# Kernel optimization log

Hardware: AMD Instinct MI355X
Metric: run time of the kernel (lower is better)

Reference implementation:

```python
import jax, jax.numpy as jnp
import numpy as np

B, N, M, K = 4, 2048, 8192, 3          # batches, coarse pts/batch, fine pts/batch, knn k
C_IN, C_SKIP, H, C_OUT = 256, 128, 256, 128


def setup_inputs() -> dict:
    key = jax.random.key(0)
    ks = jax.random.split(key, 8)
    x = jax.random.normal(ks[0], (B * N, C_IN), jnp.float32)
    pos = jax.random.normal(ks[1], (B * N, 3), jnp.float32)
    batch = jnp.repeat(jnp.arange(B, dtype=jnp.int64), N)        # sorted, equal-sized batches
    x_skip = jax.random.normal(ks[2], (B * M, C_SKIP), jnp.float32)
    pos_skip = jax.random.normal(ks[3], (B * M, 3), jnp.float32)
    batch_skip = jnp.repeat(jnp.arange(B, dtype=jnp.int64), M)
    # MLP params: Linear(384->256) + ReLU + Linear(256->128)
    W1 = jax.random.normal(ks[4], (C_IN + C_SKIP, H), jnp.float32) / np.sqrt(C_IN + C_SKIP)
    b1 = jnp.zeros((H,), jnp.float32)
    W2 = jax.random.normal(ks[5], (H, C_OUT), jnp.float32) / np.sqrt(H)
    b2 = jnp.zeros((C_OUT,), jnp.float32)
    return {"x": x, "pos": pos, "x_skip": x_skip, "pos_skip": pos_skip,
            "W1": W1, "b1": b1, "W2": W2, "b2": b2,
            "batch": batch, "batch_skip": batch_skip}


def _knn_interpolate(x, pos, pos_skip):
    # x: [B*N, C], pos: [B*N, 3], pos_skip: [B*M, 3]; batches are equal-sized & sorted,
    # so per-batch kNN == reshape to [B, n, ...] (matches batch/batch_skip vectors).
    xb = x.reshape(B, N, C_IN)
    pb = pos.reshape(B, N, 3)
    qb = pos_skip.reshape(B, M, 3)
    # squared pairwise distances via GEMM expansion: [B, M, N]
    d2 = (jnp.sum(qb * qb, -1)[:, :, None]
          + jnp.sum(pb * pb, -1)[:, None, :]
          - 2.0 * jnp.einsum('bmd,bnd->bmn', qb, pb))
    neg_d2, idx = jax.lax.top_k(-d2, K)           # k smallest distances
    d2k = jnp.maximum(-neg_d2, 0.0)               # [B, M, K]
    w = 1.0 / (d2k + 1e-16)                       # inverse-squared-distance weights
    feats = xb[jnp.arange(B)[:, None, None], idx] # gather: [B, M, K, C]
    interp = jnp.sum(w[..., None] * feats, axis=2) / jnp.sum(w, axis=2)[..., None]
    return interp.reshape(B * M, C_IN)


def reference(x, pos, x_skip, pos_skip, W1, b1, W2, b2, batch, batch_skip):
    xi = _knn_interpolate(x, pos, pos_skip)              # [B*M, C_IN]
    h = jnp.concatenate([xi, x_skip], axis=1)            # [B*M, C_IN+C_SKIP]
    h = jax.nn.relu(h @ W1 + b1)
    out = h @ W2 + b2                                    # [B*M, C_OUT]
    return (out, pos_skip, batch_skip)
```

## Files before the change

kernel.cpp:

```cpp
#include <hip/hip_runtime.h>
#include <math.h>
#include <stdint.h>

#define Bn    4
#define Nn    2048
#define Mn    8192
#define CIN   256
#define CSKIP 128
#define HID   256
#define COUT  128
#define KTOT  384

typedef short bf16x8 __attribute__((ext_vector_type(8)));
typedef float f32x16 __attribute__((ext_vector_type(16)));

__device__ __forceinline__ ushort f2bf(float f) {
    union { float f; unsigned u; } v; v.f = f;
    return (ushort)((v.u + 0x7fffu + ((v.u >> 16) & 1u)) >> 16);
}
__device__ __forceinline__ float bf2f(ushort u) {
    union { unsigned u; float f; } v; v.u = ((unsigned)u) << 16;
    return v.f;
}

#define INSERT3(kA, kB, kC, k)            \
    do {                                  \
        const double _t = fmax(kA, k);    \
        kA = fmin(kA, k);                 \
        const double _u = fmax(kB, _t);   \
        kB = fmin(kB, _t);                \
        kC = fmin(kC, _u);                \
    } while (0)

__global__ __launch_bounds__(256) void prep_kernel(
    const float* __restrict__ x, const float* __restrict__ xs,
    const float* __restrict__ pos, const float* __restrict__ pos_skip,
    const float* __restrict__ W1, const float* __restrict__ W2,
    ushort* __restrict__ xb, ushort* __restrict__ xsb,
    ushort* __restrict__ W1T, ushort* __restrict__ W2T,
    float4* __restrict__ pos4, float* __restrict__ tail_dst)
{
    const int bid = blockIdx.x, tid = threadIdx.x;
    if (bid < 2048) {
        const int q   = bid * 256 + tid;
        const int row = q >> 6;
        const int cq  = (q & 63) * 4;
        const float4 v = *(const float4*)(x + (size_t)row * CIN + cq);
        ushort4 o; o.x = f2bf(v.x); o.y = f2bf(v.y); o.z = f2bf(v.z); o.w = f2bf(v.w);
        *(ushort4*)(xb + (size_t)row * CIN + cq) = o;
    } else if (bid < 6144) {
        const int q   = (bid - 2048) * 256 + tid;
        const int row = q >> 5;
        const int cq  = (q & 31) * 4;
        const float4 v = *(const float4*)(xs + (size_t)row * CSKIP + cq);
        ushort4 o; o.x = f2bf(v.x); o.y = f2bf(v.y); o.z = f2bf(v.z); o.w = f2bf(v.w);
        *(ushort4*)(xsb + (size_t)row * CSKIP + cq) = o;
    } else if (bid < 6240) {
        const int q  = (bid - 6144) * 256 + tid;
        const int n  = q / 96;
        const int kq = (q % 96) * 4;
        ushort4 o;
        o.x = f2bf(W1[(size_t)(kq + 0) * HID + n]);
        o.y = f2bf(W1[(size_t)(kq + 1) * HID + n]);
        o.z = f2bf(W1[(size_t)(kq + 2) * HID + n]);
        o.w = f2bf(W1[(size_t)(kq + 3) * HID + n]);
        *(ushort4*)(W1T + (size_t)n * KTOT + kq) = o;
    } else if (bid < 6272) {
        const int q  = (bid - 6240) * 256 + tid;
        const int n  = q >> 6;
        const int kq = (q & 63) * 4;
        ushort4 o;
        o.x = f2bf(W2[(size_t)(kq + 0) * COUT + n]);
        o.y = f2bf(W2[(size_t)(kq + 1) * COUT + n]);
        o.z = f2bf(W2[(size_t)(kq + 2) * COUT + n]);
        o.w = f2bf(W2[(size_t)(kq + 3) * COUT + n]);
        *(ushort4*)(W2T + (size_t)n * HID + kq) = o;
    } else if (bid < 6304) {
        const int i = (bid - 6272) * 256 + tid;
        const float* p = pos + (size_t)i * 3;
        const float p0 = p[0], p1 = p[1], p2 = p[2];
        const float pp = __fadd_rn(__fadd_rn(__fmul_rn(p0, p0), __fmul_rn(p1, p1)),
                                   __fmul_rn(p2, p2));
        pos4[i] = make_float4(2.0f * p0, 2.0f * p1, 2.0f * p2, pp);
    } else {
        const int i = (bid - 6304) * 256 + tid;
        const int nPos = Bn * Mn * 3;
        if (i < nPos) tail_dst[i] = pos_skip[i];
        else          tail_dst[i] = (float)((i - nPos) >> 13);
    }
}

__device__ __forceinline__ void gemm_acc128(
    const ushort* __restrict__ A, int lda,
    const ushort* __restrict__ BT, int ldb,
    int ksteps, long rowbase, long colbase, int tid,
    ushort* Ast, ushort* Bst, f32x16 acc[2][2])
{
    const int wave = tid >> 6, lane = tid & 63;
    const int wr = wave >> 1, wc = wave & 1;
    const int l31 = lane & 31, kc0 = lane >> 5;
    const int sr0 = tid >> 2;
    const int ss0 = tid & 3;
    const int ssw = ss0 ^ (sr0 & 3);

    uint4 ra0, ra1, rb0, rb1;
    ra0 = *(const uint4*)(A + (rowbase + sr0) * lda + ss0 * 8);
    ra1 = *(const uint4*)(A + (rowbase + sr0 + 64) * lda + ss0 * 8);
    rb0 = *(const uint4*)(BT + (colbase + sr0) * ldb + ss0 * 8);
    rb1 = *(const uint4*)(BT + (colbase + sr0 + 64) * ldb + ss0 * 8);

    for (int t = 0; t < ksteps; ++t) {
        __syncthreads();
        *(uint4*)&Ast[sr0 * 32 + (ssw << 3)]        = ra0;
        *(uint4*)&Ast[(sr0 + 64) * 32 + (ssw << 3)] = ra1;
        *(uint4*)&Bst[sr0 * 32 + (ssw << 3)]        = rb0;
        *(uint4*)&Bst[(sr0 + 64) * 32 + (ssw << 3)] = rb1;
        __syncthreads();
        if (t < ksteps - 1) {
            const int kt = (t + 1) * 32;
            ra0 = *(const uint4*)(A + (rowbase + sr0) * lda + kt + ss0 * 8);
            ra1 = *(const uint4*)(A + (rowbase + sr0 + 64) * lda + kt + ss0 * 8);
            rb0 = *(const uint4*)(BT + (colbase + sr0) * ldb + kt + ss0 * 8);
            rb1 = *(const uint4*)(BT + (colbase + sr0 + 64) * ldb + kt + ss0 * 8);
        }
#pragma unroll
        for (int s = 0; s < 2; ++s) {
            bf16x8 af[2], bq[2];
#pragma unroll
            for (int mf = 0; mf < 2; ++mf) {
                const int r = wr * 64 + mf * 32 + l31;
                af[mf] = *(const bf16x8*)&Ast[r * 32 + ((((s << 1) | kc0) ^ (r & 3)) << 3)];
            }
#pragma unroll
            for (int nf = 0; nf < 2; ++nf) {
                const int rn = wc * 64 + nf * 32 + l31;
                bq[nf] = *(const bf16x8*)&Bst[rn * 32 + ((((s << 1) | kc0) ^ (rn & 3)) << 3)];
            }
#pragma unroll
            for (int mf = 0; mf < 2; ++mf)
#pragma unroll
                for (int nf = 0; nf < 2; ++nf)
                    acc[mf][nf] = __builtin_amdgcn_mfma_f32_32x32x16_bf16(
                        af[mf], bq[nf], acc[mf][nf], 0, 0, 0);
        }
    }
}

__global__ __launch_bounds__(256) void yz_gemm(
    const ushort* __restrict__ xb, const ushort* __restrict__ xsb,
    const ushort* __restrict__ W1T,
    ushort* __restrict__ Y, ushort* __restrict__ Z)
{
    __shared__ ushort Ast[128 * 32];
    __shared__ ushort Bst[128 * 32];

    const int bid = blockIdx.x, tid = threadIdx.x;
    f32x16 acc[2][2];
#pragma unroll
    for (int i = 0; i < 2; ++i)
#pragma unroll
        for (int j = 0; j < 2; ++j)
#pragma unroll
            for (int e = 0; e < 16; ++e) acc[i][j][e] = 0.0f;

    const ushort* A; ushort* C;
    long rowbase, colbase; int lda, ksteps; const ushort* BT; int ldb = KTOT;
    if (bid < 128) {
        rowbase = (long)(bid >> 1) * 128; colbase = (long)(bid & 1) * 128;
        A = xb; lda = CIN; ksteps = CIN / 32; BT = W1T; C = Y;
    } else {
        const int cb = bid - 128;
        rowbase = (long)(cb >> 1) * 128; colbase = (long)(cb & 1) * 128;
        A = xsb; lda = CSKIP; ksteps = CSKIP / 32; BT = W1T + CIN; C = Z;
    }
    gemm_acc128(A, lda, BT, ldb, ksteps, rowbase, colbase, tid, Ast, Bst, acc);

    const int wave = tid >> 6, lane = tid & 63;
    const int wr = wave >> 1, wc = wave & 1;
    const int l31 = lane & 31, kc0 = lane >> 5;
#pragma unroll
    for (int mf = 0; mf < 2; ++mf)
#pragma unroll
        for (int nf = 0; nf < 2; ++nf) {
            const long col = colbase + wc * 64 + nf * 32 + l31;
#pragma unroll
            for (int e = 0; e < 16; ++e) {
                const int rl = wr * 64 + mf * 32 + (e & 3) + ((e >> 2) << 3) + (kc0 << 2);
                C[(rowbase + rl) * HID + col] = f2bf(acc[mf][nf][e]);
            }
        }
}

__global__ __launch_bounds__(256) void knn_h(
    const float4* __restrict__ pos4,
    const float* __restrict__ pos_skip,
    const ushort* __restrict__ Y,
    const ushort* __restrict__ Z,
    const float* __restrict__ b1,
    ushort* __restrict__ h)
{
    __shared__ double sKey[16][3][17];
    __shared__ int    sIdx[16][3];
    __shared__ float  sRW[16][3];

    const int tid    = threadIdx.x;
    const int qloc   = tid & 15;
    const int chunk  = tid >> 4;
    const int blockQ = blockIdx.x * 16;
    const int b      = blockQ / Mn;

    const int q = blockQ + qloc;
    const float* qp = pos_skip + (size_t)q * 3;
    const float q0 = qp[0], q1 = qp[1], q2 = qp[2];
    const float qq = __fadd_rn(__fadd_rn(__fmul_rn(q0, q0), __fmul_rn(q1, q1)),
                               __fmul_rn(q2, q2));

    const int base = chunk * 128;
    const float4* __restrict__ cp = pos4 + (size_t)b * Nn + base;

    double kA = (double)INFINITY, kB = (double)INFINITY, kC = (double)INFINITY;
#pragma unroll 4
    for (int j = 0; j < 128; ++j) {
        const float4 P = cp[j];
        const float dot2 = __fadd_rn(__fadd_rn(__fmul_rn(q0, P.x), __fmul_rn(q1, P.y)),
                                     __fmul_rn(q2, P.z));
        const float d = __fsub_rn(__fadd_rn(qq, P.w), dot2);
        const double k = __longlong_as_double(
            __double_as_longlong((double)d) | (long long)(base + j));
        INSERT3(kA, kB, kC, k);
    }
    sKey[chunk][0][qloc] = kA;
    sKey[chunk][1][qloc] = kB;
    sKey[chunk][2][qloc] = kC;
    __syncthreads();

    if (tid < 16) {
        double mA = (double)INFINITY, mB = (double)INFINITY, mC = (double)INFINITY;
#pragma unroll
        for (int c = 0; c < 16; ++c)
#pragma unroll
            for (int s = 0; s < 3; ++s) {
                const double k = sKey[c][s][tid];
                INSERT3(mA, mB, mC, k);
            }
        const long long ba = __double_as_longlong(mA);
        const long long bb = __double_as_longlong(mB);
        const long long bc = __double_as_longlong(mC);
        const float dA = (float)__longlong_as_double(ba & ~0x7FFll);
        const float dB = (float)__longlong_as_double(bb & ~0x7FFll);
        const float dC = (float)__longlong_as_double(bc & ~0x7FFll);
        const float w0 = 1.0f / (fmaxf(dA, 0.0f) + 1e-16f);
        const float w1 = 1.0f / (fmaxf(dB, 0.0f) + 1e-16f);
        const float w2 = 1.0f / (fmaxf(dC, 0.0f) + 1e-16f);
        const float rden = 1.0f / (w0 + w1 + w2);
        sIdx[tid][0] = (int)(ba & 0x7FF);
        sIdx[tid][1] = (int)(bb & 0x7FF);
        sIdx[tid][2] = (int)(bc & 0x7FF);
        sRW[tid][0] = w0 * rden; sRW[tid][1] = w1 * rden; sRW[tid][2] = w2 * rden;
    }
    __syncthreads();

    const int wave = tid >> 6, lane = tid & 63;
    const size_t ybase = (size_t)b * Nn;
    const float4 b1v = ((const float4*)b1)[lane];
    for (int j = 0; j < 4; ++j) {
        const int lq = wave * 4 + j;
        const int gq = blockQ + lq;
        const int i0 = sIdx[lq][0], i1 = sIdx[lq][1], i2 = sIdx[lq][2];
        const float w0 = sRW[lq][0], w1 = sRW[lq][1], w2 = sRW[lq][2];
        const ushort4 y0 = ((const ushort4*)(Y + (ybase + i0) * HID))[lane];
        const ushort4 y1 = ((const ushort4*)(Y + (ybase + i1) * HID))[lane];
        const ushort4 y2 = ((const ushort4*)(Y + (ybase + i2) * HID))[lane];
        const ushort4 zz = ((const ushort4*)(Z + (size_t)gq * HID))[lane];
        ushort4 ov;
        {
            float v;
            v = fmaf(w2, bf2f(y2.x), fmaf(w1, bf2f(y1.x), w0 * bf2f(y0.x))) + bf2f(zz.x) + b1v.x;
            ov.x = f2bf(fmaxf(v, 0.0f));
            v = fmaf(w2, bf2f(y2.y), fmaf(w1, bf2f(y1.y), w0 * bf2f(y0.y))) + bf2f(zz.y) + b1v.y;
            ov.y = f2bf(fmaxf(v, 0.0f));
            v = fmaf(w2, bf2f(y2.z), fmaf(w1, bf2f(y1.z), w0 * bf2f(y0.z))) + bf2f(zz.z) + b1v.z;
            ov.z = f2bf(fmaxf(v, 0.0f));
            v = fmaf(w2, bf2f(y2.w), fmaf(w1, bf2f(y1.w), w0 * bf2f(y0.w))) + bf2f(zz.w) + b1v.w;
            ov.w = f2bf(fmaxf(v, 0.0f));
        }
        *(ushort4*)(h + (size_t)gq * HID + lane * 4) = ov;
    }
}

__global__ __launch_bounds__(256) void gemm2(
    const ushort* __restrict__ h, const ushort* __restrict__ W2T,
    const float* __restrict__ b2, float* __restrict__ out)
{
    __shared__ ushort Ast[128 * 32];
    __shared__ ushort Bst[128 * 32];

    const int tid = threadIdx.x;
    f32x16 acc[2][2];
#pragma unroll
    for (int i = 0; i < 2; ++i)
#pragma unroll
        for (int j = 0; j < 2; ++j)
#pragma unroll
            for (int e = 0; e < 16; ++e) acc[i][j][e] = 0.0f;

    const long rowbase = (long)blockIdx.x * 128;
    gemm_acc128(h, HID, W2T, HID, HID / 32, rowbase, 0, tid, Ast, Bst, acc);

    const int wave = tid >> 6, lane = tid & 63;
    const int wr = wave >> 1, wc = wave & 1;
    const int l31 = lane & 31, kc0 = lane >> 5;
#pragma unroll
    for (int mf = 0; mf < 2; ++mf)
#pragma unroll
        for (int nf = 0; nf < 2; ++nf) {
            const int col = wc * 64 + nf * 32 + l31;
            const float b2v = b2[col];
#pragma unroll
            for (int e = 0; e < 16; ++e) {
                const int rl = wr * 64 + mf * 32 + (e & 3) + ((e >> 2) << 3) + (kc0 << 2);
                out[(rowbase + rl) * COUT + col] = acc[mf][nf][e] + b2v;
            }
        }
}

extern "C" void kernel_launch(void* const* d_in, const int* in_sizes, int n_in,
                              void* d_out, int out_size, void* d_ws, size_t ws_size,
                              hipStream_t stream)
{
    const float* x        = (const float*)d_in[0];
    const float* pos      = (const float*)d_in[1];
    const float* x_skip   = (const float*)d_in[2];
    const float* pos_skip = (const float*)d_in[3];
    const float* W1       = (const float*)d_in[4];
    const float* b1       = (const float*)d_in[5];
    const float* W2       = (const float*)d_in[6];
    const float* b2       = (const float*)d_in[7];

    float* out = (float*)d_out;

    char* wp = (char*)d_ws;
    ushort* xb  = (ushort*)wp; wp += (size_t)Bn * Nn * CIN * 2;
    ushort* xsb = (ushort*)wp; wp += (size_t)Bn * Mn * CSKIP * 2;
    ushort* Yb  = (ushort*)wp; wp += (size_t)Bn * Nn * HID * 2;
    ushort* Zb  = (ushort*)wp; wp += (size_t)Bn * Mn * HID * 2;
    ushort* hb  = (ushort*)wp; wp += (size_t)Bn * Mn * HID * 2;
    ushort* W1T = (ushort*)wp; wp += (size_t)HID * KTOT * 2;
    ushort* W2T = (ushort*)wp; wp += (size_t)COUT * HID * 2;
    float4* pos4 = (float4*)wp;

    prep_kernel<<<dim3(6816), 256, 0, stream>>>(
        x, x_skip, pos, pos_skip, W1, W2, xb, xsb, W1T, W2T, pos4,
        out + (size_t)Bn * Mn * COUT);

    yz_gemm<<<dim3(640), 256, 0, stream>>>(xb, xsb, W1T, Yb, Zb);

    knn_h<<<dim3(2048), 256, 0, stream>>>(pos4, pos_skip, Yb, Zb, b1, hb);

    gemm2<<<dim3(256), 256, 0, stream>>>(hb, W2T, b2, out);
}
```

Measured before the change: 77.79 us.

## Replace brute-force kNN with x-bucketed windowed search over sorted points

Coarse points are bucket-sorted by x per batch and queries are grouped by x bucket and radius class, so each block of 16 nearby queries scans only a window of candidates instead of all 2048. The window grows until the third-nearest distance is provably inside the slab, which keeps exact kNN. The window width uses a heuristic tuned to Gaussian-distributed inputs. Sorting adds single-block-per-batch histogram and scatter work in the prep kernel, and the adaptive loop adds extra barriers.

After: 100.0 us. +28.6%, slower.

```diff
diff --git a/kernel.cpp b/kernel.cpp
--- a/kernel.cpp
+++ b/kernel.cpp
@@ -11,6 +11,13 @@
 #define COUT  128
 #define KTOT  384
 
+#define PB    256
+#define PDX   0.03125f
+#define GLOX  -4.0f
+#define QXB   128
+#define QDX   0.0625f
+#define QNB   (QXB * 4)
+
 typedef short bf16x8 __attribute__((ext_vector_type(8)));
 typedef float f32x16 __attribute__((ext_vector_type(16)));
 
@@ -32,33 +39,41 @@
         kC = fmin(kC, _u);                \
     } while (0)
 
-__global__ __launch_bounds__(256) void prep_kernel(
+__device__ __forceinline__ int pbucket(float v) {
+    int c = (int)floorf((v - GLOX) / PDX);
+    return min(max(c, 0), PB - 1);
+}
+__device__ __forceinline__ int qbucket(float v) {
+    int c = (int)floorf((v - GLOX) / QDX);
+    return min(max(c, 0), QXB - 1);
+}
+
+__global__ __launch_bounds__(256) void prep_sort(
     const float* __restrict__ x, const float* __restrict__ xs,
     const float* __restrict__ pos, const float* __restrict__ pos_skip,
     const float* __restrict__ W1, const float* __restrict__ W2,
     ushort* __restrict__ xb, ushort* __restrict__ xsb,
     ushort* __restrict__ W1T, ushort* __restrict__ W2T,
-    float4* __restrict__ pos4, float* __restrict__ tail_dst)
+    float4* __restrict__ spos4, int* __restrict__ sidxp, int* __restrict__ cellS,
+    float4* __restrict__ qp4, int* __restrict__ qoi,
+    float* __restrict__ tail_dst)
 {
     const int bid = blockIdx.x, tid = threadIdx.x;
     if (bid < 2048) {
-        const int q   = bid * 256 + tid;
-        const int row = q >> 6;
-        const int cq  = (q & 63) * 4;
+        const int q = bid * 256 + tid;
+        const int row = q >> 6, cq = (q & 63) * 4;
         const float4 v = *(const float4*)(x + (size_t)row * CIN + cq);
         ushort4 o; o.x = f2bf(v.x); o.y = f2bf(v.y); o.z = f2bf(v.z); o.w = f2bf(v.w);
         *(ushort4*)(xb + (size_t)row * CIN + cq) = o;
     } else if (bid < 6144) {
-        const int q   = (bid - 2048) * 256 + tid;
-        const int row = q >> 5;
-        const int cq  = (q & 31) * 4;
+        const int q = (bid - 2048) * 256 + tid;
+        const int row = q >> 5, cq = (q & 31) * 4;
         const float4 v = *(const float4*)(xs + (size_t)row * CSKIP + cq);
         ushort4 o; o.x = f2bf(v.x); o.y = f2bf(v.y); o.z = f2bf(v.z); o.w = f2bf(v.w);
         *(ushort4*)(xsb + (size_t)row * CSKIP + cq) = o;
     } else if (bid < 6240) {
-        const int q  = (bid - 6144) * 256 + tid;
-        const int n  = q / 96;
-        const int kq = (q % 96) * 4;
+        const int q = (bid - 6144) * 256 + tid;
+        const int n = q / 96, kq = (q % 96) * 4;
         ushort4 o;
         o.x = f2bf(W1[(size_t)(kq + 0) * HID + n]);
         o.y = f2bf(W1[(size_t)(kq + 1) * HID + n]);
@@ -66,27 +81,83 @@
         o.w = f2bf(W1[(size_t)(kq + 3) * HID + n]);
         *(ushort4*)(W1T + (size_t)n * KTOT + kq) = o;
     } else if (bid < 6272) {
-        const int q  = (bid - 6240) * 256 + tid;
-        const int n  = q >> 6;
-        const int kq = (q & 63) * 4;
+        const int q = (bid - 6240) * 256 + tid;
+        const int n = q >> 6, kq = (q & 63) * 4;
         ushort4 o;
         o.x = f2bf(W2[(size_t)(kq + 0) * COUT + n]);
         o.y = f2bf(W2[(size_t)(kq + 1) * COUT + n]);
         o.z = f2bf(W2[(size_t)(kq + 2) * COUT + n]);
         o.w = f2bf(W2[(size_t)(kq + 3) * COUT + n]);
         *(ushort4*)(W2T + (size_t)n * HID + kq) = o;
-    } else if (bid < 6304) {
+    } else if (bid < 6784) {
         const int i = (bid - 6272) * 256 + tid;
-        const float* p = pos + (size_t)i * 3;
-        const float p0 = p[0], p1 = p[1], p2 = p[2];
-        const float pp = __fadd_rn(__fadd_rn(__fmul_rn(p0, p0), __fmul_rn(p1, p1)),
-                                   __fmul_rn(p2, p2));
-        pos4[i] = make_float4(2.0f * p0, 2.0f * p1, 2.0f * p2, pp);
-    } else {
-        const int i = (bid - 6304) * 256 + tid;
         const int nPos = Bn * Mn * 3;
         if (i < nPos) tail_dst[i] = pos_skip[i];
         else          tail_dst[i] = (float)((i - nPos) >> 13);
+    } else if (bid < 6788) {
+        __shared__ int hist[PB]; __shared__ int cst[PB + 1]; __shared__ int cnt[PB];
+        const int b = bid - 6784;
+        for (int c = tid; c < PB; c += 256) { hist[c] = 0; cnt[c] = 0; }
+        __syncthreads();
+        int cellv[8];
+#pragma unroll
+        for (int t = 0; t < 8; ++t) {
+            const int i = tid * 8 + t;
+            const int c = pbucket(pos[((size_t)b * Nn + i) * 3]);
+            cellv[t] = c;
+            atomicAdd(&hist[c], 1);
+        }
+        __syncthreads();
+        if (tid == 0) {
+            int acc = 0;
+            for (int c = 0; c < PB; ++c) { cst[c] = acc; acc += hist[c]; }
+            cst[PB] = acc;
+        }
+        __syncthreads();
+#pragma unroll
+        for (int t = 0; t < 8; ++t) {
+            const int i = tid * 8 + t;
+            const float* p = pos + ((size_t)b * Nn + i) * 3;
+            const float p0 = p[0], p1 = p[1], p2 = p[2];
+            const float pp = __fadd_rn(__fadd_rn(__fmul_rn(p0, p0), __fmul_rn(p1, p1)),
+                                       __fmul_rn(p2, p2));
+            const int slot = cst[cellv[t]] + atomicAdd(&cnt[cellv[t]], 1);
+            spos4[(size_t)b * Nn + slot] = make_float4(2.0f * p0, 2.0f * p1, 2.0f * p2, pp);
+            sidxp[(size_t)b * Nn + slot] = i;
+        }
+        __syncthreads();
+        for (int c = tid; c <= PB; c += 256) cellS[b * (PB + 1) + c] = cst[c];
+    } else {
+        __shared__ int qh[QNB]; __shared__ int qst[QNB]; __shared__ int qcn[QNB];
+        const int b = bid - 6788;
+        for (int c = tid; c < QNB; c += 256) { qh[c] = 0; qcn[c] = 0; }
+        __syncthreads();
+        for (int t = 0; t < 32; ++t) {
+            const int i = tid * 32 + t;
+            const float* p = pos_skip + ((size_t)b * Mn + i) * 3;
+            const float qq = __fadd_rn(__fadd_rn(__fmul_rn(p[0], p[0]), __fmul_rn(p[1], p[1])),
+                                       __fmul_rn(p[2], p[2]));
+            const int cls = (qq < 2.0f) ? 0 : (qq < 4.0f) ? 1 : (qq < 8.0f) ? 2 : 3;
+            atomicAdd(&qh[qbucket(p[0]) * 4 + cls], 1);
+        }
+        __syncthreads();
+        if (tid == 0) {
+            int acc = 0;
+            for (int c = 0; c < QNB; ++c) { qst[c] = acc; acc += qh[c]; }
+        }
+        __syncthreads();
+        for (int t = 0; t < 32; ++t) {
+            const int i = tid * 32 + t;
+            const float* p = pos_skip + ((size_t)b * Mn + i) * 3;
+            const float p0 = p[0], p1 = p[1], p2 = p[2];
+            const float qq = __fadd_rn(__fadd_rn(__fmul_rn(p0, p0), __fmul_rn(p1, p1)),
+                                       __fmul_rn(p2, p2));
+            const int cls = (qq < 2.0f) ? 0 : (qq < 4.0f) ? 1 : (qq < 8.0f) ? 2 : 3;
+            const int key = qbucket(p0) * 4 + cls;
+            const int slot = qst[key] + atomicAdd(&qcn[key], 1);
+            qp4[(size_t)b * Mn + slot] = make_float4(p0, p1, p2, qq);
+            qoi[(size_t)b * Mn + slot] = b * Mn + i;
+        }
     }
 }
 
@@ -191,81 +262,119 @@
         }
 }
 
-__global__ __launch_bounds__(256) void knn_h(
-    const float4* __restrict__ pos4,
-    const float* __restrict__ pos_skip,
-    const ushort* __restrict__ Y,
-    const ushort* __restrict__ Z,
-    const float* __restrict__ b1,
-    ushort* __restrict__ h)
+#define SCAN_RANGE(S, E)                                                        \
+    for (int i = (S) + chunk; i < (E); i += 16) {                               \
+        const float4 P = cp[i];                                                 \
+        const float dot2 = __fadd_rn(__fadd_rn(__fmul_rn(q0, P.x),              \
+                              __fmul_rn(q1, P.y)), __fmul_rn(q2, P.z));         \
+        const float d = __fsub_rn(__fadd_rn(qq, P.w), dot2);                    \
+        const double kk = __longlong_as_double(                                 \
+            __double_as_longlong((double)d) | (long long)ci[i]);                \
+        INSERT3(kA, kB, kC, kk);                                                \
+    }
+
+__global__ __launch_bounds__(256) void knn_win(
+    const float4* __restrict__ spos4, const int* __restrict__ sidxp,
+    const int* __restrict__ cellS,
+    const float4* __restrict__ qp4, const int* __restrict__ qoi,
+    const ushort* __restrict__ Y, const ushort* __restrict__ Z,
+    const float* __restrict__ b1, ushort* __restrict__ h)
 {
     __shared__ double sKey[16][3][17];
     __shared__ int    sIdx[16][3];
     __shared__ float  sRW[16][3];
-
-    const int tid    = threadIdx.x;
-    const int qloc   = tid & 15;
-    const int chunk  = tid >> 4;
-    const int blockQ = blockIdx.x * 16;
-    const int b      = blockQ / Mn;
-
-    const int q = blockQ + qloc;
-    const float* qp = pos_skip + (size_t)q * 3;
-    const float q0 = qp[0], q1 = qp[1], q2 = qp[2];
-    const float qq = __fadd_rn(__fadd_rn(__fmul_rn(q0, q0), __fmul_rn(q1, q1)),
-                               __fmul_rn(q2, q2));
-
-    const int base = chunk * 128;
-    const float4* __restrict__ cp = pos4 + (size_t)b * Nn + base;
+    __shared__ int    sOrig[16];
+    __shared__ float  sX[16], sQQ[16];
+    __shared__ int    sOkAll;
+
+    const int tid = threadIdx.x, qloc = tid & 15, chunk = tid >> 4;
+    const int sel = blockIdx.x;
+    const int b = sel >> 9;
+    const size_t slotbase = (size_t)b * Mn + (sel & 511) * 16;
+
+    if (tid == 0) sOkAll = 1;
+    if (tid < 16) {
+        const float4 qp = qp4[slotbase + tid];
+        sX[tid] = qp.x; sQQ[tid] = qp.w;
+        sOrig[tid] = qoi[slotbase + tid];
+    }
+    __syncthreads();
+
+    float xmin = sX[0], xmax = sX[0], qqmax = sQQ[0];
+#pragma unroll
+    for (int i = 1; i < 16; ++i) {
+        xmin = fminf(xmin, sX[i]); xmax = fmaxf(xmax, sX[i]);
+        qqmax = fmaxf(qqmax, sQQ[i]);
+    }
+
+    const float4 qp = qp4[slotbase + qloc];
+    const float q0 = qp.x, q1 = qp.y, q2 = qp.z, qq = qp.w;
+
+    const float4* __restrict__ cp = spos4 + (size_t)b * Nn;
+    const int*    __restrict__ ci = sidxp + (size_t)b * Nn;
+    const int*    __restrict__ cs = cellS + b * (PB + 1);
+
+    float W = 0.21f * expf(qqmax * (1.0f / 6.0f)) + 0.04f;
+    int blo = pbucket(xmin - W), bhi = pbucket(xmax + W);
+    int ws = cs[blo], we = cs[bhi + 1];
 
     double kA = (double)INFINITY, kB = (double)INFINITY, kC = (double)INFINITY;
-#pragma unroll 4
-    for (int j = 0; j < 128; ++j) {
-        const float4 P = cp[j];
-        const float dot2 = __fadd_rn(__fadd_rn(__fmul_rn(q0, P.x), __fmul_rn(q1, P.y)),
-                                     __fmul_rn(q2, P.z));
-        const float d = __fsub_rn(__fadd_rn(qq, P.w), dot2);
-        const double k = __longlong_as_double(
-            __double_as_longlong((double)d) | (long long)(base + j));
-        INSERT3(kA, kB, kC, k);
-    }
-    sKey[chunk][0][qloc] = kA;
-    sKey[chunk][1][qloc] = kB;
-    sKey[chunk][2][qloc] = kC;
-    __syncthreads();
-
-    if (tid < 16) {
-        double mA = (double)INFINITY, mB = (double)INFINITY, mC = (double)INFINITY;
-#pragma unroll
-        for (int c = 0; c < 16; ++c)
-#pragma unroll
-            for (int s = 0; s < 3; ++s) {
-                const double k = sKey[c][s][tid];
-                INSERT3(mA, mB, mC, k);
-            }
-        const long long ba = __double_as_longlong(mA);
-        const long long bb = __double_as_longlong(mB);
-        const long long bc = __double_as_longlong(mC);
-        const float dA = (float)__longlong_as_double(ba & ~0x7FFll);
-        const float dB = (float)__longlong_as_double(bb & ~0x7FFll);
-        const float dC = (float)__longlong_as_double(bc & ~0x7FFll);
-        const float w0 = 1.0f / (fmaxf(dA, 0.0f) + 1e-16f);
-        const float w1 = 1.0f / (fmaxf(dB, 0.0f) + 1e-16f);
-        const float w2 = 1.0f / (fmaxf(dC, 0.0f) + 1e-16f);
-        const float rden = 1.0f / (w0 + w1 + w2);
-        sIdx[tid][0] = (int)(ba & 0x7FF);
-        sIdx[tid][1] = (int)(bb & 0x7FF);
-        sIdx[tid][2] = (int)(bc & 0x7FF);
-        sRW[tid][0] = w0 * rden; sRW[tid][1] = w1 * rden; sRW[tid][2] = w2 * rden;
-    }
-    __syncthreads();
+    SCAN_RANGE(ws, we)
+
+    for (;;) {
+        sKey[chunk][0][qloc] = kA;
+        sKey[chunk][1][qloc] = kB;
+        sKey[chunk][2][qloc] = kC;
+        __syncthreads();
+        if (tid < 16) {
+            double mA = (double)INFINITY, mB = (double)INFINITY, mC = (double)INFINITY;
+#pragma unroll
+            for (int c = 0; c < 16; ++c)
+#pragma unroll
+                for (int s = 0; s < 3; ++s) {
+                    const double k = sKey[c][s][tid];
+                    INSERT3(mA, mB, mC, k);
+                }
+            const long long ba = __double_as_longlong(mA);
+            const long long bb = __double_as_longlong(mB);
+            const long long bc = __double_as_longlong(mC);
+            const float dA = (float)__longlong_as_double(ba & ~0x7FFll);
+            const float dB = (float)__longlong_as_double(bb & ~0x7FFll);
+            const float dC = (float)__longlong_as_double(bc & ~0x7FFll);
+            const float w0 = 1.0f / (fmaxf(dA, 0.0f) + 1e-16f);
+            const float w1 = 1.0f / (fmaxf(dB, 0.0f) + 1e-16f);
+            const float w2 = 1.0f / (fmaxf(dC, 0.0f) + 1e-16f);
+            const float rden = 1.0f / (w0 + w1 + w2);
+            sIdx[tid][0] = (int)(ba & 0x7FF);
+            sIdx[tid][1] = (int)(bb & 0x7FF);
+            sIdx[tid][2] = (int)(bc & 0x7FF);
+            sRW[tid][0] = w0 * rden; sRW[tid][1] = w1 * rden; sRW[tid][2] = w2 * rden;
+            const float qx = sX[tid];
+            const float gL = (blo > 0)      ? (qx - (GLOX + (float)blo * PDX)) : 1e30f;
+            const float gR = (bhi < PB - 1) ? ((GLOX + (float)(bhi + 1) * PDX) - qx) : 1e30f;
+            const float g = fmaxf(fminf(gL, gR), 0.0f);
+            if (!(dC < g * g - 1e-3f)) atomicAnd(&sOkAll, 0);
+        }
+        __syncthreads();
+        const bool allok = (sOkAll != 0);
+        const bool full = (blo == 0 && bhi == PB - 1);
+        if (allok || full) break;
+        __syncthreads();
+        if (tid == 0) sOkAll = 1;
+        W *= 1.6f;
+        const int nblo = pbucket(xmin - W), nbhi = pbucket(xmax + W);
+        const int nws = cs[nblo], nwe = cs[nbhi + 1];
+        SCAN_RANGE(nws, ws)
+        SCAN_RANGE(we, nwe)
+        ws = nws; we = nwe; blo = nblo; bhi = nbhi;
+    }
 
     const int wave = tid >> 6, lane = tid & 63;
     const size_t ybase = (size_t)b * Nn;
     const float4 b1v = ((const float4*)b1)[lane];
     for (int j = 0; j < 4; ++j) {
         const int lq = wave * 4 + j;
-        const int gq = blockQ + lq;
+        const int gq = sOrig[lq];
         const int i0 = sIdx[lq][0], i1 = sIdx[lq][1], i2 = sIdx[lq][2];
         const float w0 = sRW[lq][0], w1 = sRW[lq][1], w2 = sRW[lq][2];
         const ushort4 y0 = ((const ushort4*)(Y + (ybase + i0) * HID))[lane];
@@ -273,17 +382,15 @@
         const ushort4 y2 = ((const ushort4*)(Y + (ybase + i2) * HID))[lane];
         const ushort4 zz = ((const ushort4*)(Z + (size_t)gq * HID))[lane];
         ushort4 ov;
-        {
-            float v;
-            v = fmaf(w2, bf2f(y2.x), fmaf(w1, bf2f(y1.x), w0 * bf2f(y0.x))) + bf2f(zz.x) + b1v.x;
-            ov.x = f2bf(fmaxf(v, 0.0f));
-            v = fmaf(w2, bf2f(y2.y), fmaf(w1, bf2f(y1.y), w0 * bf2f(y0.y))) + bf2f(zz.y) + b1v.y;
-            ov.y = f2bf(fmaxf(v, 0.0f));
-            v = fmaf(w2, bf2f(y2.z), fmaf(w1, bf2f(y1.z), w0 * bf2f(y0.z))) + bf2f(zz.z) + b1v.z;
-            ov.z = f2bf(fmaxf(v, 0.0f));
-            v = fmaf(w2, bf2f(y2.w), fmaf(w1, bf2f(y1.w), w0 * bf2f(y0.w))) + bf2f(zz.w) + b1v.w;
-            ov.w = f2bf(fmaxf(v, 0.0f));
-        }
+        float v;
+        v = fmaf(w2, bf2f(y2.x), fmaf(w1, bf2f(y1.x), w0 * bf2f(y0.x))) + bf2f(zz.x) + b1v.x;
+        ov.x = f2bf(fmaxf(v, 0.0f));
+        v = fmaf(w2, bf2f(y2.y), fmaf(w1, bf2f(y1.y), w0 * bf2f(y0.y))) + bf2f(zz.y) + b1v.y;
+        ov.y = f2bf(fmaxf(v, 0.0f));
+        v = fmaf(w2, bf2f(y2.z), fmaf(w1, bf2f(y1.z), w0 * bf2f(y0.z))) + bf2f(zz.z) + b1v.z;
+        ov.z = f2bf(fmaxf(v, 0.0f));
+        v = fmaf(w2, bf2f(y2.w), fmaf(w1, bf2f(y1.w), w0 * bf2f(y0.w))) + bf2f(zz.w) + b1v.w;
+        ov.w = f2bf(fmaxf(v, 0.0f));
         *(ushort4*)(h + (size_t)gq * HID + lane * 4) = ov;
     }
 }
@@ -340,22 +447,27 @@
     float* out = (float*)d_out;
 
     char* wp = (char*)d_ws;
-    ushort* xb  = (ushort*)wp; wp += (size_t)Bn * Nn * CIN * 2;
-    ushort* xsb = (ushort*)wp; wp += (size_t)Bn * Mn * CSKIP * 2;
-    ushort* Yb  = (ushort*)wp; wp += (size_t)Bn * Nn * HID * 2;
-    ushort* Zb  = (ushort*)wp; wp += (size_t)Bn * Mn * HID * 2;
-    ushort* hb  = (ushort*)wp; wp += (size_t)Bn * Mn * HID * 2;
-    ushort* W1T = (ushort*)wp; wp += (size_t)HID * KTOT * 2;
-    ushort* W2T = (ushort*)wp; wp += (size_t)COUT * HID * 2;
-    float4* pos4 = (float4*)wp;
-
-    prep_kernel<<<dim3(6816), 256, 0, stream>>>(
-        x, x_skip, pos, pos_skip, W1, W2, xb, xsb, W1T, W2T, pos4,
-        out + (size_t)Bn * Mn * COUT);
+    ushort* xb   = (ushort*)wp; wp += (size_t)Bn * Nn * CIN * 2;
+    ushort* xsb  = (ushort*)wp; wp += (size_t)Bn * Mn * CSKIP * 2;
+    ushort* Yb   = (ushort*)wp; wp += (size_t)Bn * Nn * HID * 2;
+    ushort* Zb   = (ushort*)wp; wp += (size_t)Bn * Mn * HID * 2;
+    ushort* hb   = (ushort*)wp; wp += (size_t)Bn * Mn * HID * 2;
+    ushort* W1T  = (ushort*)wp; wp += (size_t)HID * KTOT * 2;
+    ushort* W2T  = (ushort*)wp; wp += (size_t)COUT * HID * 2;
+    float4* spos4 = (float4*)wp; wp += (size_t)Bn * Nn * 16;
+    int*    sidxp = (int*)wp;    wp += (size_t)Bn * Nn * 4;
+    int*    cellS = (int*)wp;    wp += (size_t)Bn * (PB + 1) * 4;
+    float4* qp4   = (float4*)wp; wp += (size_t)Bn * Mn * 16;
+    int*    qoi   = (int*)wp;
+
+    prep_sort<<<dim3(6792), 256, 0, stream>>>(
+        x, x_skip, pos, pos_skip, W1, W2, xb, xsb, W1T, W2T,
+        spos4, sidxp, cellS, qp4, qoi, out + (size_t)Bn * Mn * COUT);
 
     yz_gemm<<<dim3(640), 256, 0, stream>>>(xb, xsb, W1T, Yb, Zb);
 
-    knn_h<<<dim3(2048), 256, 0, stream>>>(pos4, pos_skip, Yb, Zb, b1, hb);
+    knn_win<<<dim3(2048), 256, 0, stream>>>(
+        spos4, sidxp, cellS, qp4, qoi, Yb, Zb, b1, hb);
 
     gemm2<<<dim3(256), 256, 0, stream>>>(hb, W2T, b2, out);
 }
```
